# Kernel tuning notes

Measured on AMD Instinct MI355X. Metric: run time of the kernel, lower is better.

The kernel has to match this reference:

```python
import jax, jax.numpy as jnp
import numpy as np

B = 32768
IN_DIM, OUT_DIM, VAR_DIM = 2, 3, 50
KER_DIMS = [1024, 1024, 1024, 1024]
NSTEPS = 32  # fixed-step RK4 stand-in for adaptive odeint over t in [0, 1]


def setup_inputs() -> dict:
    key = jax.random.key(0)
    ks = jax.random.split(key, 11)
    x = jax.random.normal(ks[0], (B, IN_DIM), dtype=jnp.float32)
    dims = [VAR_DIM] + KER_DIMS + [VAR_DIM]
    inp = {"x": x}
    for i, (d1, d2) in enumerate(zip(dims[:-1], dims[1:])):
        # torch Linear(d1+1, d2): weight (d2, d1+1); stored here as (d1+1, d2)
        bound = 1.0 / np.sqrt(d1 + 1)
        inp[f"W{i}"] = jax.random.uniform(ks[1 + 2 * i], (d1 + 1, d2), jnp.float32, -bound, bound)
        inp[f"b{i}"] = jax.random.uniform(ks[2 + 2 * i], (d2,), jnp.float32, -bound, bound)
    return inp


def _odefunc(t, y, Ws, bs):
    # Each layer: concat time column, Linear, ReLU (except last) -- matches ODEfunc.forward
    out = y
    n = len(Ws)
    for i in range(n):
        tcol = jnp.full((out.shape[0], 1), t, dtype=out.dtype)
        h = jnp.concatenate([out, tcol], axis=1)
        out = h @ Ws[i] + bs[i]
        if i < n - 1:
            out = jax.nn.relu(out)
    return out


def _integrate(x, Ws, bs):
    # Pad input into var_dim state: out[:, :in_dim] = x, rest zeros
    y0 = jnp.zeros((x.shape[0], VAR_DIM), dtype=x.dtype).at[:, : x.shape[1]].set(x)
    dt = jnp.asarray(1.0 / NSTEPS, dtype=x.dtype)
    ts = jnp.arange(NSTEPS, dtype=x.dtype) * dt

    def step(y, t):
        k1 = _odefunc(t, y, Ws, bs)
        k2 = _odefunc(t + dt * 0.5, y + dt * 0.5 * k1, Ws, bs)
        k3 = _odefunc(t + dt * 0.5, y + dt * 0.5 * k2, Ws, bs)
        k4 = _odefunc(t + dt, y + dt * k3, Ws, bs)
        return y + (dt / 6.0) * (k1 + 2.0 * k2 + 2.0 * k3 + k4), None

    y1, _ = jax.lax.scan(step, y0, ts)
    return y1[:, :OUT_DIM]


def reference(x, W0, b0, W1, b1, W2, b2, W3, b3, W4, b4):
    Ws = (W0, W1, W2, W3, W4)
    bs = (b0, b1, b2, b3, b4)
    return _integrate(x, Ws, bs)
```

## Files before the change

kernel.cpp:

```cpp
#include <hip/hip_runtime.h>
#include <hip/hip_bf16.h>
#include <stdint.h>


typedef __bf16 bf16_t;
typedef bf16_t bf16x8 __attribute__((ext_vector_type(8)));
typedef float  f32x4  __attribute__((ext_vector_type(4)));

#define DEVI static __device__ __forceinline__

DEVI void gload_lds16(const bf16_t* gsrc, bf16_t* ldst) {
  __builtin_amdgcn_global_load_lds(
      (const __attribute__((address_space(1))) uint32_t*)gsrc,
      (__attribute__((address_space(3))) uint32_t*)ldst,
      16, 0, 0);
}

template<int K>
__global__ __launch_bounds__(512, 2) void gemm256(
    const bf16_t* __restrict__ A,
    const bf16_t* __restrict__ BT,
    const float* __restrict__ bias,
    const float* __restrict__ wtime,
    float t,
    bf16_t* __restrict__ C, int ldc,
    int M, int N)
{
  constexpr int NT = K / 64;
  static_assert(NT >= 2, "need >=2 K-tiles");

  __shared__ __align__(16) bf16_t As[2][256][64];
  __shared__ __align__(16) bf16_t Bs[2][256][64];

  const int tid  = threadIdx.x;
  const int wave = tid >> 6;
  const int lane = tid & 63;
  const int wr = wave >> 2;
  const int wc = wave & 3;

  int wg = blockIdx.x;
  {
    const int cpx = gridDim.x >> 3;
    wg = (wg & 7) * cpx + (wg >> 3);
  }
  const int nbn = N >> 8;
  const int bm = (wg / nbn) << 8;
  const int bn = (wg % nbn) << 8;

  const int srow = lane >> 3;
  const int scol = ((lane & 7) << 3) ^ ((lane & 32) >> 1) ^ ((wave & 1) << 5);
  const bf16_t* aS = A  + (size_t)(bm + wave * 8 + srow) * K + scol;
  const bf16_t* bS = BT + (size_t)(bn + wave * 8 + srow) * K + scol;
  bf16_t* aD = &As[0][0][0] + wave * 8 * 64;
  bf16_t* bD = &Bs[0][0][0] + wave * 8 * 64;

  auto stageHalf = [&](int kt, int isB, int h) {
    const int buf = kt & 1;
    const bf16_t* src = (isB ? bS : aS) + (size_t)(h * 128) * K + kt * 64;
    bf16_t*       dst = (isB ? bD : aD) + (buf * 256 + h * 128) * 64;
    gload_lds16(src,                  dst);
    gload_lds16(src + (size_t)64 * K, dst + 64 * 64);
  };
  auto stageTile = [&](int kt) {
    stageHalf(kt, 0, 0); stageHalf(kt, 0, 1);
    stageHalf(kt, 1, 0); stageHalf(kt, 1, 1);
  };

  const int fr = lane & 15;
  const int fq = lane >> 4;
  const int rsw = ((fr & 4) << 3) ^ ((fr & 8) << 3);

  bf16x8 ah0[8], ah1[8];
  bf16x8 bh0[4], bh1[4];
  f32x4  acc[8][4] = {};

  auto lda_into = [&](bf16x8 (&dst)[8], int buf, int mh) {
    const char* base = (const char*)&As[buf][0][0];
#pragma unroll
    for (int m = 0; m < 4; ++m)
#pragma unroll
      for (int kk = 0; kk < 2; ++kk) {
        int r  = wr * 128 + (mh * 4 + m) * 16 + fr;
        int cb = (kk * 64 + fq * 16) ^ rsw;
        dst[m * 2 + kk] = *(const bf16x8*)(base + r * 128 + cb);
      }
  };
  auto ldb_into = [&](bf16x8 (&dst)[4], int buf, int nh) {
    const char* base = (const char*)&Bs[buf][0][0];
#pragma unroll
    for (int n = 0; n < 2; ++n)
#pragma unroll
      for (int kk = 0; kk < 2; ++kk) {
        int r  = wc * 64 + (nh * 2 + n) * 16 + fr;
        int cb = (kk * 64 + fq * 16) ^ rsw;
        dst[n * 2 + kk] = *(const bf16x8*)(base + r * 128 + cb);
      }
  };
  auto mma_quad = [&](bf16x8 (&a)[8], bf16x8 (&b)[4], int mh, int nh) {
    __builtin_amdgcn_s_setprio(1);
#pragma unroll
    for (int m = 0; m < 4; ++m)
#pragma unroll
      for (int n = 0; n < 2; ++n)
#pragma unroll
        for (int kk = 0; kk < 2; ++kk)
          acc[mh * 4 + m][nh * 2 + n] = __builtin_amdgcn_mfma_f32_16x16x32_bf16(
              a[m * 2 + kk], b[n * 2 + kk],
              acc[mh * 4 + m][nh * 2 + n], 0, 0, 0);
    __builtin_amdgcn_s_setprio(0);
  };

  stageTile(0);
  asm volatile("s_waitcnt vmcnt(0)" ::: "memory");
  __builtin_amdgcn_s_barrier();
  lda_into(ah0, 0, 0);
  ldb_into(bh0, 0, 0);

  for (int t2 = 0; t2 < NT; ++t2) {
    const int buf = t2 & 1;
    if (t2 + 1 < NT) stageTile(t2 + 1);
    ldb_into(bh1, buf, 1);
    mma_quad(ah0, bh0, 0, 0);
    lda_into(ah1, buf, 1);
    mma_quad(ah0, bh1, 0, 1);
    mma_quad(ah1, bh0, 1, 0);
    if (t2 + 1 < NT) {
      asm volatile("s_waitcnt vmcnt(0)" ::: "memory");
      __builtin_amdgcn_s_barrier();
      lda_into(ah0, buf ^ 1, 0);
      ldb_into(bh0, buf ^ 1, 0);
    }
    mma_quad(ah1, bh1, 1, 1);
  }

#pragma unroll
  for (int n = 0; n < 4; ++n) {
    const int gcol = bn + wc * 64 + n * 16 + fr;
    const float bv = bias[gcol] + t * wtime[gcol];
#pragma unroll
    for (int m = 0; m < 8; ++m) {
      const int grow0 = bm + wr * 128 + m * 16 + (fq << 2);
#pragma unroll
      for (int r = 0; r < 4; ++r) {
        float v = acc[m][n][r] + bv;
        v = v > 0.0f ? v : 0.0f;
        C[(size_t)(grow0 + r) * ldc + gcol] = (bf16_t)v;
      }
    }
  }
}

template<int BM, int BN, int BK, int WROWS, int WCOLS, bool RELU, bool OUT_BF16>
__global__ __launch_bounds__(256) void gemm_bt(
    const bf16_t* __restrict__ A, int lda,
    const bf16_t* __restrict__ BT,
    const float* __restrict__ bias,
    const float* __restrict__ wtime,
    float t,
    void* __restrict__ Cv, int ldc,
    int M, int K)
{
  static_assert(BK == 64, "swizzle assumes BK=64");
  constexpr int MR  = BM / WROWS / 16;
  constexpr int NR  = BN / WCOLS / 16;
  constexpr int TPR = BK / 8;
  constexpr int RPW = 64 / TPR;
  constexpr int RPL = 4 * RPW;
  static_assert(BM % RPL == 0 && BN % RPL == 0, "tile staging mismatch");

  __shared__ bf16_t As[BM][BK];
  __shared__ bf16_t Bs[BN][BK];

  const int tid  = threadIdx.x;
  const int wave = tid >> 6;
  const int lane = tid & 63;
  const int wr = wave / WCOLS;
  const int wc = wave % WCOLS;
  const int bm = blockIdx.x * BM;
  const int bn = blockIdx.y * BN;
  const int lrow = lane >> 3;
  const int lcol = (((lane & 7) << 3) ^ ((lane & 32) >> 1) ^ ((wave & 1) << 5));

  const int fr = lane & 15;
  const int fq = lane >> 4;
  const int esw = ((fr & 4) << 2) ^ ((fr & 8) << 2);

  f32x4 acc[MR][NR] = {};

  for (int k0 = 0; k0 < K; k0 += BK) {
#pragma unroll
    for (int i = 0; i < BM / RPL; ++i) {
      const int rb = i * RPL + wave * RPW;
      gload_lds16(&A[(size_t)(bm + rb + lrow) * lda + k0 + lcol], &As[rb][0]);
    }
#pragma unroll
    for (int i = 0; i < BN / RPL; ++i) {
      const int rb = i * RPL + wave * RPW;
      gload_lds16(&BT[(size_t)(bn + rb + lrow) * K + k0 + lcol], &Bs[rb][0]);
    }
    __syncthreads();
#pragma unroll
    for (int kk = 0; kk < BK / 32; ++kk) {
      bf16x8 af[MR], bfr[NR];
      const int ecol = (kk * 32 + fq * 8) ^ esw;
#pragma unroll
      for (int m = 0; m < MR; ++m)
        af[m] = *(const bf16x8*)&As[wr * (BM / WROWS) + m * 16 + fr][ecol];
#pragma unroll
      for (int n = 0; n < NR; ++n)
        bfr[n] = *(const bf16x8*)&Bs[wc * (BN / WCOLS) + n * 16 + fr][ecol];
#pragma unroll
      for (int m = 0; m < MR; ++m)
#pragma unroll
        for (int n = 0; n < NR; ++n)
          acc[m][n] = __builtin_amdgcn_mfma_f32_16x16x32_bf16(
              af[m], bfr[n], acc[m][n], 0, 0, 0);
    }
    __syncthreads();
  }

#pragma unroll
  for (int n = 0; n < NR; ++n) {
    const int gcol = bn + wc * (BN / WCOLS) + n * 16 + fr;
    const float bv = bias[gcol] + t * wtime[gcol];
#pragma unroll
    for (int m = 0; m < MR; ++m) {
      const int grow0 = bm + wr * (BM / WROWS) + m * 16 + (fq << 2);
#pragma unroll
      for (int r = 0; r < 4; ++r) {
        float v = acc[m][n][r] + bv;
        if (RELU) v = v > 0.0f ? v : 0.0f;
        if constexpr (OUT_BF16)
          ((bf16_t*)Cv)[(size_t)(grow0 + r) * ldc + gcol] = (bf16_t)v;
        else
          ((float*)Cv)[(size_t)(grow0 + r) * ldc + gcol] = v;
      }
    }
  }
}

__global__ __launch_bounds__(256) void gemm_l4_rk4_l0(
    const bf16_t* __restrict__ A, int lda,
    const bf16_t* __restrict__ BT,
    const float* __restrict__ bias,
    const float* __restrict__ wtime,
    float t,
    const bf16_t* __restrict__ BT0,
    const float* __restrict__ bias0,
    const float* __restrict__ wtime0,
    float tn,
    float* __restrict__ y, float* __restrict__ accb,
    bf16_t* __restrict__ act0,
    float ca, float cs, int mode,
    int M, int K)
{
  constexpr int MR = 2, NR = 2;
  const int NT = K / 64;

  __shared__ __align__(16) bf16_t As[2][64][64];
  __shared__ __align__(16) bf16_t Bs[2][64][64];
  __shared__ bf16_t Ys[64][72];

  const int tid  = threadIdx.x;
  const int wave = tid >> 6;
  const int lane = tid & 63;
  const int wr = wave >> 1;
  const int wc = wave & 1;
  const int bm = blockIdx.x * 64;
  const int lrow = lane >> 3;
  const int lcol = (((lane & 7) << 3) ^ ((lane & 32) >> 1) ^ ((wave & 1) << 5));

  const bf16_t* aS = A  + (size_t)(bm + wave * 8 + lrow) * lda + lcol;
  const bf16_t* bS = BT + (size_t)(wave * 8 + lrow) * K + lcol;
  bf16_t* aD = &As[0][0][0] + wave * 8 * 64;
  bf16_t* bD = &Bs[0][0][0] + wave * 8 * 64;

  auto stage = [&](int kt) {
    const int buf = kt & 1;
    gload_lds16(aS + kt * 64,                      aD + buf * 64 * 64);
    gload_lds16(aS + (size_t)32 * lda + kt * 64,   aD + buf * 64 * 64 + 32 * 64);
    gload_lds16(bS + kt * 64,                      bD + buf * 64 * 64);
    gload_lds16(bS + (size_t)32 * K + kt * 64,     bD + buf * 64 * 64 + 32 * 64);
  };

  const int fr = lane & 15;
  const int fq = lane >> 4;
  const int esw = ((fr & 4) << 2) ^ ((fr & 8) << 2);

  bf16x8 af0[2], af1[2], bf0[2], bf1[2];
  f32x4 acc[MR][NR] = {};

  auto ldaf = [&](bf16x8 (&d)[2], int buf, int kk) {
    const int ecol = (kk * 32 + fq * 8) ^ esw;
#pragma unroll
    for (int m = 0; m < 2; ++m)
      d[m] = *(const bf16x8*)&As[buf][wr * 32 + m * 16 + fr][ecol];
  };
  auto ldbf = [&](bf16x8 (&d)[2], int buf, int kk) {
    const int ecol = (kk * 32 + fq * 8) ^ esw;
#pragma unroll
    for (int n = 0; n < 2; ++n)
      d[n] = *(const bf16x8*)&Bs[buf][wc * 32 + n * 16 + fr][ecol];
  };
  auto mma = [&](bf16x8 (&a)[2], bf16x8 (&b)[2]) {
#pragma unroll
    for (int m = 0; m < 2; ++m)
#pragma unroll
      for (int n = 0; n < 2; ++n)
        acc[m][n] = __builtin_amdgcn_mfma_f32_16x16x32_bf16(
            a[m], b[n], acc[m][n], 0, 0, 0);
  };

  stage(0);
  asm volatile("s_waitcnt vmcnt(0)" ::: "memory");
  __builtin_amdgcn_s_barrier();
  ldaf(af0, 0, 0);
  ldbf(bf0, 0, 0);

  for (int t2 = 0; t2 < NT; ++t2) {
    const int buf = t2 & 1;
    if (t2 + 1 < NT) stage(t2 + 1);
    ldaf(af1, buf, 1);
    ldbf(bf1, buf, 1);
    mma(af0, bf0);
    if (t2 + 1 < NT) {
      asm volatile("s_waitcnt vmcnt(0)" ::: "memory");
      __builtin_amdgcn_s_barrier();
      ldaf(af0, buf ^ 1, 0);
      ldbf(bf0, buf ^ 1, 0);
    }
    mma(af1, bf1);
  }

#pragma unroll
  for (int n = 0; n < NR; ++n) {
    const int gcol = wc * 32 + n * 16 + fr;
    const float bv = bias[gcol] + t * wtime[gcol];
#pragma unroll
    for (int m = 0; m < MR; ++m) {
      const int lr0 = wr * 32 + m * 16 + (fq << 2);
#pragma unroll
      for (int r = 0; r < 4; ++r) {
        const float kv = acc[m][n][r] + bv;
        const size_t o = (size_t)(bm + lr0 + r) * 64 + gcol;
        float yb;
        if (mode == 0) {
          accb[o] = kv;
          yb = y[o] + cs * kv;
        } else if (mode == 1) {
          accb[o] += ca * kv;
          yb = y[o] + cs * kv;
        } else {
          const float ny = y[o] + cs * (accb[o] + kv);
          y[o] = ny;
          yb = ny;
        }
        Ys[lr0 + r][gcol] = (bf16_t)yb;
      }
    }
  }
  __syncthreads();

  const int colbase = wave * 256;
  bf16x8 af0v[4][2];
#pragma unroll
  for (int m2 = 0; m2 < 4; ++m2)
#pragma unroll
    for (int kk = 0; kk < 2; ++kk)
      af0v[m2][kk] = *(const bf16x8*)&Ys[m2 * 16 + fr][kk * 32 + fq * 8];

  bf16x8 bfA[4][2], bfB[4][2];
  auto ldb0 = [&](bf16x8 (&d)[4][2], int g) {
#pragma unroll
    for (int n = 0; n < 4; ++n)
#pragma unroll
      for (int kk = 0; kk < 2; ++kk)
        d[n][kk] = *(const bf16x8*)(BT0
            + (size_t)(colbase + g * 64 + n * 16 + fr) * 64 + kk * 32 + fq * 8);
  };
  ldb0(bfA, 0);

#pragma unroll
  for (int g = 0; g < 4; ++g) {
    bf16x8 (&bcur)[4][2]  = (g & 1) ? bfB : bfA;
    bf16x8 (&bnext)[4][2] = (g & 1) ? bfA : bfB;
    if (g + 1 < 4) ldb0(bnext, g + 1);
    f32x4 acc2[4][4] = {};
#pragma unroll
    for (int kk = 0; kk < 2; ++kk)
#pragma unroll
      for (int m2 = 0; m2 < 4; ++m2)
#pragma unroll
        for (int n = 0; n < 4; ++n)
          acc2[m2][n] = __builtin_amdgcn_mfma_f32_16x16x32_bf16(
              af0v[m2][kk], bcur[n][kk], acc2[m2][n], 0, 0, 0);
#pragma unroll
    for (int n = 0; n < 4; ++n) {
      const int col = colbase + g * 64 + n * 16 + fr;
      const float bv = bias0[col] + tn * wtime0[col];
#pragma unroll
      for (int m2 = 0; m2 < 4; ++m2) {
        const int row0 = bm + m2 * 16 + (fq << 2);
#pragma unroll
        for (int r = 0; r < 4; ++r) {
          float v = acc2[m2][n][r] + bv;
          v = v > 0.0f ? v : 0.0f;
          act0[(size_t)(row0 + r) * 1024 + col] = (bf16_t)v;
        }
      }
    }
  }
}

__global__ void prep_weight(const float* __restrict__ W, const float* __restrict__ b,
                            bf16_t* __restrict__ WT, float* __restrict__ bias,
                            float* __restrict__ wtime,
                            int K, int N, int Kpad, int Npad)
{
  int idx = blockIdx.x * 256 + threadIdx.x;
  int total = Npad * Kpad;
  if (idx < total) {
    int n = idx / Kpad, k = idx % Kpad;
    float v = (n < N && k < K) ? W[(size_t)k * N + n] : 0.0f;
    WT[idx] = (bf16_t)v;
  }
  if (idx < Npad) {
    bias[idx]  = (idx < N) ? b[idx] : 0.0f;
    wtime[idx] = (idx < N) ? W[(size_t)K * N + idx] : 0.0f;
  }
}

__global__ void init_y(const float* __restrict__ x, float* __restrict__ y,
                       bf16_t* __restrict__ ybf, int M)
{
  int i = blockIdx.x * 256 + threadIdx.x;
  if (i < M * 64) {
    int m = i >> 6, c = i & 63;
    float v = (c < 2) ? x[m * 2 + c] : 0.0f;
    y[i] = v;
    ybf[i] = (bf16_t)v;
  }
}

__global__ void extract_out(const float* __restrict__ y, float* __restrict__ out, int M)
{
  int i = blockIdx.x * 256 + threadIdx.x;
  if (i < M * 3) {
    int m = i / 3, c = i % 3;
    out[i] = y[(size_t)m * 64 + c];
  }
}

extern "C" void kernel_launch(void* const* d_in, const int* in_sizes, int n_in,
                              void* d_out, int out_size, void* d_ws, size_t ws_size,
                              hipStream_t stream)
{
  (void)in_sizes; (void)n_in; (void)out_size; (void)ws_size;
  const int M = 32768;

  const float* x = (const float*)d_in[0];
  const float* Wp[5]; const float* bp[5];
  for (int i = 0; i < 5; ++i) {
    Wp[i] = (const float*)d_in[1 + 2 * i];
    bp[i] = (const float*)d_in[2 + 2 * i];
  }

  char* ws = (char*)d_ws; size_t off = 0;
  auto alloc = [&](size_t bytes) -> char* {
    char* p = ws + off; off += (bytes + 255) & ~(size_t)255; return p;
  };

  bf16_t* WT[5];
  WT[0] = (bf16_t*)alloc((size_t)1024 * 64 * 2);
  WT[1] = (bf16_t*)alloc((size_t)1024 * 1024 * 2);
  WT[2] = (bf16_t*)alloc((size_t)1024 * 1024 * 2);
  WT[3] = (bf16_t*)alloc((size_t)1024 * 1024 * 2);
  WT[4] = (bf16_t*)alloc((size_t)64 * 1024 * 2);
  float* bias[5]; float* wtm[5];
  for (int i = 0; i < 5; ++i) {
    int Np = (i == 4) ? 64 : 1024;
    bias[i] = (float*)alloc((size_t)Np * 4);
    wtm[i]  = (float*)alloc((size_t)Np * 4);
  }
  float*  y    = (float*)alloc((size_t)M * 64 * 4);
  float*  accb = (float*)alloc((size_t)M * 64 * 4);
  bf16_t* ybf  = (bf16_t*)alloc((size_t)M * 64 * 2);
  bf16_t* act0 = (bf16_t*)alloc((size_t)M * 1024 * 2);
  bf16_t* act1 = (bf16_t*)alloc((size_t)M * 1024 * 2);

  const int Kd[5]  = {50, 1024, 1024, 1024, 1024};
  const int Nd[5]  = {1024, 1024, 1024, 1024, 50};
  const int Kpd[5] = {64, 1024, 1024, 1024, 1024};
  const int Npd[5] = {1024, 1024, 1024, 1024, 64};
  for (int i = 0; i < 5; ++i) {
    int tot = Npd[i] * Kpd[i];
    prep_weight<<<dim3((tot + 255) / 256), 256, 0, stream>>>(
        Wp[i], bp[i], WT[i], bias[i], wtm[i], Kd[i], Nd[i], Kpd[i], Npd[i]);
  }

  init_y<<<dim3((M * 64 + 255) / 256), 256, 0, stream>>>(x, y, ybf, M);

  const float dtv = 1.0f / 32.0f;
  dim3 gL0(M / 128, 1024 / 128);
  dim3 g256(M / 256 * (1024 / 256));
  dim3 gL4(M / 64);

  gemm_bt<128,128,64,2,2,true,true><<<gL0, 256, 0, stream>>>(
      ybf, 64, WT[0], bias[0], wtm[0], 0.0f, act0, 1024, M, 64);

  auto run_eval = [&](float t, float tn, float ca, float cs, int mode) {
    gemm256<1024><<<g256, 512, 0, stream>>>(
        act0, WT[1], bias[1], wtm[1], t, act1, 1024, M, 1024);
    gemm256<1024><<<g256, 512, 0, stream>>>(
        act1, WT[2], bias[2], wtm[2], t, act0, 1024, M, 1024);
    gemm256<1024><<<g256, 512, 0, stream>>>(
        act0, WT[3], bias[3], wtm[3], t, act1, 1024, M, 1024);
    gemm_l4_rk4_l0<<<gL4, 256, 0, stream>>>(
        act1, 1024, WT[4], bias[4], wtm[4], t,
        WT[0], bias[0], wtm[0], tn,
        y, accb, act0, ca, cs, mode, M, 1024);
  };

  for (int i = 0; i < 32; ++i) {
    const float t0 = i * dtv;
    const float tm = t0 + 0.5f * dtv;
    const float t1 = t0 + dtv;
    const float t0n = (i + 1) * dtv;
    run_eval(t0, tm,  0.0f, 0.5f * dtv, 0);
    run_eval(tm, tm,  2.0f, 0.5f * dtv, 1);
    run_eval(tm, t1,  2.0f, dtv,        1);
    run_eval(t1, t0n, 0.0f, dtv / 6.0f, 2);
  }

  extract_out<<<dim3((M * 3 + 255) / 256), 256, 0, stream>>>(y, (float*)d_out, M);
}
```

Measured before the change: 33.63 ms.

## Switch GEMM to 32-wide K tiles with triple-buffered LDS and two-deep prefetch

The GEMM main loop now uses 32-wide K tiles and a three-slot LDS ring instead of 64-wide tiles in two buffers. Global-to-LDS loads run two tiles ahead, paced by partial vmcnt waits, and fragments for the next tile are read from LDS while MFMAs run on the current one. The goal is to hide global load latency better and shrink the LDS footprint. In exchange there are twice as many barriers per K, and the fixed vmcnt(4) wait on the final iteration may not cover the last tile's loads, which risks a race.

```diff
diff --git a/kernel.cpp b/kernel.cpp
--- a/kernel.cpp
+++ b/kernel.cpp
@@ -26,11 +26,11 @@
     bf16_t* __restrict__ C, int ldc,
     int M, int N)
 {
-  constexpr int NT = K / 64;
-  static_assert(NT >= 2, "need >=2 K-tiles");
-
-  __shared__ __align__(16) bf16_t As[2][256][64];
-  __shared__ __align__(16) bf16_t Bs[2][256][64];
+  constexpr int NT = K / 32;
+  static_assert(NT >= 4 && (NT % 2) == 0, "pipeline needs even NT >= 4");
+
+  __shared__ __align__(16) bf16_t As[3][256][32];
+  __shared__ __align__(16) bf16_t Bs[3][256][32];
 
   const int tid  = threadIdx.x;
   const int wave = tid >> 6;
@@ -47,90 +47,78 @@
   const int bm = (wg / nbn) << 8;
   const int bn = (wg % nbn) << 8;
 
-  const int srow = lane >> 3;
-  const int scol = ((lane & 7) << 3) ^ ((lane & 32) >> 1) ^ ((wave & 1) << 5);
-  const bf16_t* aS = A  + (size_t)(bm + wave * 8 + srow) * K + scol;
-  const bf16_t* bS = BT + (size_t)(bn + wave * 8 + srow) * K + scol;
-  bf16_t* aD = &As[0][0][0] + wave * 8 * 64;
-  bf16_t* bD = &Bs[0][0][0] + wave * 8 * 64;
-
-  auto stageHalf = [&](int kt, int isB, int h) {
-    const int buf = kt & 1;
-    const bf16_t* src = (isB ? bS : aS) + (size_t)(h * 128) * K + kt * 64;
-    bf16_t*       dst = (isB ? bD : aD) + (buf * 256 + h * 128) * 64;
-    gload_lds16(src,                  dst);
-    gload_lds16(src + (size_t)64 * K, dst + 64 * 64);
-  };
-  auto stageTile = [&](int kt) {
-    stageHalf(kt, 0, 0); stageHalf(kt, 0, 1);
-    stageHalf(kt, 1, 0); stageHalf(kt, 1, 1);
-  };
-
-  const int fr = lane & 15;
-  const int fq = lane >> 4;
-  const int rsw = ((fr & 4) << 3) ^ ((fr & 8) << 3);
-
-  bf16x8 ah0[8], ah1[8];
-  bf16x8 bh0[4], bh1[4];
+  const int srow   = lane >> 2;
+  const int schunk = (lane & 3) ^ ((lane >> 3) & 3);
+  const int scol   = schunk << 3;
+  const bf16_t* aS = A  + (size_t)(bm + wave * 16 + srow) * K + scol;
+  const bf16_t* bS = BT + (size_t)(bn + wave * 16 + srow) * K + scol;
+  bf16_t* aD = &As[0][0][0] + wave * 16 * 32;
+  bf16_t* bD = &Bs[0][0][0] + wave * 16 * 32;
+
+  auto stage = [&](int kt) {
+    const int buf = kt % 3;
+    const bf16_t* sa = aS + kt * 32;
+    const bf16_t* sb = bS + kt * 32;
+    bf16_t* da = aD + buf * 256 * 32;
+    bf16_t* db = bD + buf * 256 * 32;
+    gload_lds16(sa,                   da);
+    gload_lds16(sa + (size_t)128 * K, da + 128 * 32);
+    gload_lds16(sb,                   db);
+    gload_lds16(sb + (size_t)128 * K, db + 128 * 32);
+  };
+
+  const int fr  = lane & 15;
+  const int fq  = lane >> 4;
+  const int rsw = ((fr >> 1) & 3) << 4;
+
+  bf16x8 afA[8], bfA[4], afB[8], bfB[4];
   f32x4  acc[8][4] = {};
 
-  auto lda_into = [&](bf16x8 (&dst)[8], int buf, int mh) {
-    const char* base = (const char*)&As[buf][0][0];
-#pragma unroll
-    for (int m = 0; m < 4; ++m)
-#pragma unroll
-      for (int kk = 0; kk < 2; ++kk) {
-        int r  = wr * 128 + (mh * 4 + m) * 16 + fr;
-        int cb = (kk * 64 + fq * 16) ^ rsw;
-        dst[m * 2 + kk] = *(const bf16x8*)(base + r * 128 + cb);
-      }
-  };
-  auto ldb_into = [&](bf16x8 (&dst)[4], int buf, int nh) {
-    const char* base = (const char*)&Bs[buf][0][0];
-#pragma unroll
-    for (int n = 0; n < 2; ++n)
-#pragma unroll
-      for (int kk = 0; kk < 2; ++kk) {
-        int r  = wc * 64 + (nh * 2 + n) * 16 + fr;
-        int cb = (kk * 64 + fq * 16) ^ rsw;
-        dst[n * 2 + kk] = *(const bf16x8*)(base + r * 128 + cb);
-      }
-  };
-  auto mma_quad = [&](bf16x8 (&a)[8], bf16x8 (&b)[4], int mh, int nh) {
+  auto ldfrags = [&](bf16x8 (&a)[8], bf16x8 (&b)[4], int kt) {
+    const int buf = kt % 3;
+    const char* ab = (const char*)&As[buf][0][0];
+    const char* bb = (const char*)&Bs[buf][0][0];
+    const int cb = (fq * 16) ^ rsw;
+#pragma unroll
+    for (int m = 0; m < 8; ++m) {
+      const int r = wr * 128 + m * 16 + fr;
+      a[m] = *(const bf16x8*)(ab + r * 64 + cb);
+    }
+#pragma unroll
+    for (int n = 0; n < 4; ++n) {
+      const int r = wc * 64 + n * 16 + fr;
+      b[n] = *(const bf16x8*)(bb + r * 64 + cb);
+    }
+  };
+  auto mma_tile = [&](bf16x8 (&a)[8], bf16x8 (&b)[4]) {
     __builtin_amdgcn_s_setprio(1);
 #pragma unroll
-    for (int m = 0; m < 4; ++m)
-#pragma unroll
-      for (int n = 0; n < 2; ++n)
-#pragma unroll
-        for (int kk = 0; kk < 2; ++kk)
-          acc[mh * 4 + m][nh * 2 + n] = __builtin_amdgcn_mfma_f32_16x16x32_bf16(
-              a[m * 2 + kk], b[n * 2 + kk],
-              acc[mh * 4 + m][nh * 2 + n], 0, 0, 0);
+    for (int m = 0; m < 8; ++m)
+#pragma unroll
+      for (int n = 0; n < 4; ++n)
+        acc[m][n] = __builtin_amdgcn_mfma_f32_16x16x32_bf16(
+            a[m], b[n], acc[m][n], 0, 0, 0);
     __builtin_amdgcn_s_setprio(0);
   };
 
-  stageTile(0);
-  asm volatile("s_waitcnt vmcnt(0)" ::: "memory");
+  stage(0); stage(1);
+  asm volatile("s_waitcnt vmcnt(4)" ::: "memory");
   __builtin_amdgcn_s_barrier();
-  lda_into(ah0, 0, 0);
-  ldb_into(bh0, 0, 0);
-
-  for (int t2 = 0; t2 < NT; ++t2) {
-    const int buf = t2 & 1;
-    if (t2 + 1 < NT) stageTile(t2 + 1);
-    ldb_into(bh1, buf, 1);
-    mma_quad(ah0, bh0, 0, 0);
-    lda_into(ah1, buf, 1);
-    mma_quad(ah0, bh1, 0, 1);
-    mma_quad(ah1, bh0, 1, 0);
-    if (t2 + 1 < NT) {
-      asm volatile("s_waitcnt vmcnt(0)" ::: "memory");
-      __builtin_amdgcn_s_barrier();
-      lda_into(ah0, buf ^ 1, 0);
-      ldb_into(bh0, buf ^ 1, 0);
-    }
-    mma_quad(ah1, bh1, 1, 1);
+  ldfrags(afA, bfA, 0);
+
+  for (int t2 = 0; t2 < NT; t2 += 2) {
+    if (t2 + 2 < NT) stage(t2 + 2);
+    asm volatile("s_waitcnt vmcnt(4)" ::: "memory");
+    asm volatile("s_waitcnt lgkmcnt(0)" ::: "memory");
+    __builtin_amdgcn_s_barrier();
+    if (t2 + 1 < NT) ldfrags(afB, bfB, t2 + 1);
+    mma_tile(afA, bfA);
+    if (t2 + 3 < NT) stage(t2 + 3);
+    asm volatile("s_waitcnt vmcnt(4)" ::: "memory");
+    asm volatile("s_waitcnt lgkmcnt(0)" ::: "memory");
+    __builtin_amdgcn_s_barrier();
+    if (t2 + 2 < NT) ldfrags(afA, bfA, t2 + 2);
+    mma_tile(afB, bfB);
   }
 
 #pragma unroll
```

Measured after the change: 33.89 ms. No clear change (+0.8%).
